# Performance work log

Hardware: AMD Instinct MI355X
Metric: run time of the kernel (lower is better)

The kernel has to match this reference:

```python
import jax, jax.numpy as jnp
import numpy as np

EMBED = 1024
HEADS = 16
HD = EMBED // HEADS
FF = 4096
EPS = 1e-5

def _layernorm(x, g, b):
    mu = jnp.mean(x, axis=-1, keepdims=True)
    var = jnp.mean(jnp.square(x - mu), axis=-1, keepdims=True)
    return (x - mu) * jax.lax.rsqrt(var + EPS) * g + b

def setup_inputs() -> dict:
    key = jax.random.key(0)
    ks = jax.random.split(key, 10)
    s = 0.02
    return {
        "x": jax.random.normal(ks[0], (4, 2048, EMBED), dtype=jnp.float32),
        "Wq": jax.random.normal(ks[1], (EMBED, EMBED), dtype=jnp.float32) * s,
        "Wk": jax.random.normal(ks[2], (EMBED, EMBED), dtype=jnp.float32) * s,
        "Wv": jax.random.normal(ks[3], (EMBED, EMBED), dtype=jnp.float32) * s,
        "Wo": jax.random.normal(ks[4], (EMBED, EMBED), dtype=jnp.float32) * s,
        "bo": jnp.zeros((EMBED,), dtype=jnp.float32),
        "W1": jax.random.normal(ks[5], (EMBED, FF), dtype=jnp.float32) * s,
        "b1": jnp.zeros((FF,), dtype=jnp.float32),
        "W2": jax.random.normal(ks[6], (FF, EMBED), dtype=jnp.float32) * s,
        "b2": jnp.zeros((EMBED,), dtype=jnp.float32),
        "g1": jnp.ones((EMBED,), dtype=jnp.float32),
        "be1": jnp.zeros((EMBED,), dtype=jnp.float32),
        "g2": jnp.ones((EMBED,), dtype=jnp.float32),
        "be2": jnp.zeros((EMBED,), dtype=jnp.float32),
    }

def reference(x, Wq, Wk, Wv, Wo, bo, W1, b1, W2, b2, g1, be1, g2, be2):
    B, T, _ = x.shape
    # --- pre-norm self-attention (dropout = identity in eval) ---
    h = _layernorm(x, g1, be1)
    q = (h @ Wq).reshape(B, T, HEADS, HD).transpose(0, 2, 1, 3)  # bhtd
    k = (h @ Wk).reshape(B, T, HEADS, HD).transpose(0, 2, 1, 3)
    v = (h @ Wv).reshape(B, T, HEADS, HD).transpose(0, 2, 1, 3)
    scores = jnp.einsum('bhid,bhjd->bhij', q, k) / jnp.sqrt(jnp.float32(HD))
    causal = jnp.tril(jnp.ones((T, T), dtype=bool))
    scores = jnp.where(causal[None, None], scores, -jnp.inf)
    attn = jax.nn.softmax(scores, axis=-1)
    out = jnp.einsum('bhij,bhjd->bhid', attn, v)
    out = out.transpose(0, 2, 1, 3).reshape(B, T, EMBED)
    out = out @ Wo + bo
    x = x + out
    # --- pre-norm GELU FFN ---
    h2 = _layernorm(x, g2, be2)
    ff = jax.nn.gelu(h2 @ W1 + b1, approximate=False) @ W2 + b2
    return x + ff
```

## Files before the change

kernel.cpp:

```cpp
#include <hip/hip_runtime.h>

typedef unsigned short u16;
typedef __attribute__((ext_vector_type(8))) short bf16x8;
typedef __attribute__((ext_vector_type(4))) float f32x4;

#define EMBED 1024
#define FFDIM 4096
#define SEQ   2048
#define NTOK  8192
#define ATT_C 0.18033688011112042f

__device__ __forceinline__ u16 f2bf(float f) {
  union { float f; unsigned int u; } c; c.f = f;
  unsigned int r = ((c.u >> 16) & 1u) + 0x7fffu;
  return (u16)((c.u + r) >> 16);
}

__device__ __forceinline__ unsigned cvtpk(float lo, float hi) {
  unsigned r;
  asm("v_cvt_pk_bf16_f32 %0, %1, %2" : "=v"(r) : "v"(lo), "v"(hi));
  return r;
}

__device__ __forceinline__ void gload16(const u16* g, u16* l) {
  __builtin_amdgcn_global_load_lds((const __attribute__((address_space(1))) void*)g,
                                   (__attribute__((address_space(3))) void*)l, 16, 0, 0);
}

__global__ __launch_bounds__(256) void wtrans(const float* __restrict__ W,
                                              u16* __restrict__ Wt, int K, int N) {
  __shared__ float tile[32][33];
  const int tx = threadIdx.x & 31, ty = threadIdx.x >> 5;
  const int n0 = blockIdx.x << 5, k0 = blockIdx.y << 5;
#pragma unroll
  for (int r = 0; r < 32; r += 8)
    tile[ty + r][tx] = W[(size_t)(k0 + ty + r) * N + n0 + tx];
  __syncthreads();
#pragma unroll
  for (int r = 0; r < 32; r += 8)
    Wt[(size_t)(n0 + ty + r) * K + k0 + tx] = f2bf(tile[tx][ty + r]);
}

__global__ __launch_bounds__(256) void vtrans(const u16* __restrict__ qkv,
                                              u16* __restrict__ Vt) {
  __shared__ u16 tile[32][33];
  const int tx = threadIdx.x & 31, ty = threadIdx.x >> 5;
  const int t0 = blockIdx.x << 5;
  const int rg0 = blockIdx.y << 5;
  const int bh = rg0 >> 6, d0 = rg0 & 63;
  const int b = bh >> 4, h = bh & 15;
#pragma unroll
  for (int r = 0; r < 32; r += 8)
    tile[ty + r][tx] = qkv[(size_t)(b * SEQ + t0 + ty + r) * 3072 + 2048 + h * 64 + d0 + tx];
  __syncthreads();
#pragma unroll
  for (int r = 0; r < 32; r += 8)
    Vt[(size_t)(rg0 + ty + r) * SEQ + t0 + tx] = tile[tx][ty + r];
}

__global__ __launch_bounds__(256) void ln_kernel(const float* __restrict__ xin,
                                                 const float* __restrict__ gamma,
                                                 const float* __restrict__ beta,
                                                 u16* __restrict__ out) {
  const int row = blockIdx.x, tid = threadIdx.x;
  const float4 v = reinterpret_cast<const float4*>(xin + (size_t)row * EMBED)[tid];
  float s  = v.x + v.y + v.z + v.w;
  float ss = v.x * v.x + v.y * v.y + v.z * v.z + v.w * v.w;
#pragma unroll
  for (int m = 1; m < 64; m <<= 1) { s += __shfl_xor(s, m); ss += __shfl_xor(ss, m); }
  __shared__ float red[8];
  if ((tid & 63) == 0) { red[tid >> 6] = s; red[4 + (tid >> 6)] = ss; }
  __syncthreads();
  s  = red[0] + red[1] + red[2] + red[3];
  ss = red[4] + red[5] + red[6] + red[7];
  const float mean = s * (1.0f / EMBED);
  const float var  = ss * (1.0f / EMBED) - mean * mean;
  const float rstd = rsqrtf(var + 1e-5f);
  const float4 g  = reinterpret_cast<const float4*>(gamma)[tid];
  const float4 bb = reinterpret_cast<const float4*>(beta)[tid];
  ushort4 o;
  o.x = f2bf((v.x - mean) * rstd * g.x + bb.x);
  o.y = f2bf((v.y - mean) * rstd * g.y + bb.y);
  o.z = f2bf((v.z - mean) * rstd * g.z + bb.z);
  o.w = f2bf((v.w - mean) * rstd * g.w + bb.w);
  reinterpret_cast<ushort4*>(out + (size_t)row * EMBED)[tid] = o;
}

template <int NREP, int EPI>
__global__ __launch_bounds__(512, 2) void gemm4(const u16* __restrict__ A,
                                                const u16* __restrict__ Bt,
                                                void* __restrict__ Cv,
                                                const float* __restrict__ bias,
                                                const float* __restrict__ res,
                                                int M, int N, int K) {
  constexpr int BN = NREP * 64;
  constexpr int G0 = 4;
  constexpr int G1 = (NREP == 4) ? 4 : 3;
  constexpr int G3 = (NREP == 4) ? 4 : 3;
  constexpr int GP = (NREP == 4) ? 4 : 3;
  __shared__ __align__(16) u16 As[2][256 * 64];
  __shared__ __align__(16) u16 Bs[2][BN * 64];

  const int tid = threadIdx.x;
  const int lane = tid & 63, wid = tid >> 6;
  const int l4 = lane >> 4, l15 = lane & 15;
  const int wq = wid >> 2, wn = wid & 3;

  const int gx = gridDim.x;
  const int nwg = gx * (int)gridDim.y;
  const int flat = (int)blockIdx.y * gx + (int)blockIdx.x;
  const int cpx = nwg >> 3;
  const int swz = (flat & 7) * cpx + (flat >> 3);
  const int brow = (swz / gx) << 8;
  const int bcol = (swz % gx) * BN;

  const f32x4 z4 = {0.f, 0.f, 0.f, 0.f};
  f32x4 acc[4][4][NREP / 2];
#pragma unroll
  for (int q = 0; q < 4; ++q)
#pragma unroll
    for (int m = 0; m < 4; ++m)
#pragma unroll
      for (int n = 0; n < NREP / 2; ++n) acc[q][m][n] = z4;

  const int srow = tid >> 3;
  const int scolb = ((tid & 7) << 4) ^ ((srow & 7) << 4);
  const u16* gAs = A  + (size_t)(brow + srow) * K + (scolb >> 1);
  const u16* gBs = Bt + (size_t)(bcol + srow) * K + (scolb >> 1);
  const int lA = wid * 512;

  const int nk = K >> 6;

#define STAGE_A(c_, t_, h_)                                                     \
  do {                                                                          \
    gload16(gAs + (size_t)((h_) * 128) * K + (size_t)(t_) * 64,                 \
            &As[c_][(h_) * 8192 + lA]);                                         \
    gload16(gAs + (size_t)((h_) * 128 + 64) * K + (size_t)(t_) * 64,            \
            &As[c_][(h_) * 8192 + 4096 + lA]);                                  \
  } while (0)
#define STAGE_B(c_, t_, h_)                                                     \
  do {                                                                          \
    if constexpr (NREP == 4) {                                                  \
      gload16(gBs + (size_t)((h_) * 128) * K + (size_t)(t_) * 64,               \
              &Bs[c_][(h_) * 8192 + lA]);                                       \
      gload16(gBs + (size_t)((h_) * 128 + 64) * K + (size_t)(t_) * 64,          \
              &Bs[c_][(h_) * 8192 + 4096 + lA]);                                \
    } else {                                                                    \
      gload16(gBs + (size_t)((h_) * 64) * K + (size_t)(t_) * 64,                \
              &Bs[c_][(h_) * 4096 + lA]);                                       \
    }                                                                           \
  } while (0)

#define SB __builtin_amdgcn_sched_barrier(0)
#define BARR do { SB; __builtin_amdgcn_s_barrier(); SB; } while (0)
#define LG0  do { asm volatile("s_waitcnt lgkmcnt(0)" ::: "memory"); SB; } while (0)
#define VM(N_) do { asm volatile("s_waitcnt vmcnt(%0)" :: "i"(N_) : "memory"); SB; } while (0)

  const int kk0  = l4 << 3;
  const int aswz = (l15 & 7) << 3;

#define RD_A(MH)                                                                \
  _Pragma("unroll")                                                             \
  for (int m_ = 0; m_ < 4; ++m_)                                                \
    _Pragma("unroll")                                                           \
    for (int ks_ = 0; ks_ < 2; ++ks_)                                           \
      af[m_][ks_] = *(const bf16x8*)&As[c][((MH) * 128 + wq * 64 + m_ * 16 + l15) * 64 + ((kk0 + ks_ * 32) ^ aswz)];
#define RD_B(NH)                                                                \
  _Pragma("unroll")                                                             \
  for (int n_ = 0; n_ < NREP / 2; ++n_)                                         \
    _Pragma("unroll")                                                           \
    for (int ks_ = 0; ks_ < 2; ++ks_)                                           \
      bf[n_][ks_] = *(const bf16x8*)&Bs[c][((NH) * (BN / 2) + wn * (BN / 8) + n_ * 16 + l15) * 64 + ((kk0 + ks_ * 32) ^ aswz)];
#define MFMA_Q(Q_)                                                              \
  __builtin_amdgcn_s_setprio(1);                                                \
  _Pragma("unroll")                                                             \
  for (int m_ = 0; m_ < 4; ++m_)                                                \
    _Pragma("unroll")                                                           \
    for (int n_ = 0; n_ < NREP / 2; ++n_)                                       \
      _Pragma("unroll")                                                         \
      for (int ks_ = 0; ks_ < 2; ++ks_)                                         \
        acc[Q_][m_][n_] = __builtin_amdgcn_mfma_f32_16x16x32_bf16(              \
            af[m_][ks_], bf[n_][ks_], acc[Q_][m_][n_], 0, 0, 0);                \
  __builtin_amdgcn_s_setprio(0);

  bf16x8 af[4][2], bf[NREP / 2][2];

  STAGE_A(0, 0, 0);
  STAGE_B(0, 0, 0);
  STAGE_B(0, 0, 1);
  STAGE_A(0, 0, 1);
  VM(GP);
  BARR;

  for (int t = 0; t < nk - 1; ++t) {
    const int c = t & 1, cn = c ^ 1;
    RD_A(0); RD_B(0);
    STAGE_A(cn, t + 1, 0);
    BARR; LG0;
    MFMA_Q(0);
    VM(G0); BARR;
    RD_B(1);
    STAGE_B(cn, t + 1, 0);
    BARR; LG0;
    MFMA_Q(1);
    VM(G1); BARR;
    RD_A(1);
    STAGE_B(cn, t + 1, 1);
    BARR; LG0;
    MFMA_Q(2);
    BARR;
    RD_B(0);
    STAGE_A(cn, t + 1, 1);
    BARR; LG0;
    MFMA_Q(3);
    VM(G3); BARR;
  }

  {
    const int c = (nk - 1) & 1;
    RD_A(0); RD_B(0);
    BARR; LG0;
    MFMA_Q(0);
    VM(2); BARR;
    RD_B(1);
    BARR; LG0;
    MFMA_Q(1);
    VM(0); BARR;
    RD_A(1);
    BARR; LG0;
    MFMA_Q(2);
    BARR;
    RD_B(0);
    LG0;
    MFMA_Q(3);
  }

#undef STAGE_A
#undef STAGE_B
#undef SB
#undef BARR
#undef LG0
#undef VM
#undef RD_A
#undef RD_B
#undef MFMA_Q

#pragma unroll
  for (int q = 0; q < 4; ++q) {
    const int mh = q >> 1, nh = (q >> 1) ^ (q & 1);
    const int rowb = brow + mh * 128 + wq * 64 + (l4 << 2);
    const int colb = bcol + nh * (BN / 2) + wn * (BN / 8) + l15;
#pragma unroll
    for (int n = 0; n < NREP / 2; ++n) {
      const int col = colb + n * 16;
      float bv = 0.f;
      if (EPI != 0) bv = bias[col];
#pragma unroll
      for (int m = 0; m < 4; ++m) {
#pragma unroll
        for (int j = 0; j < 4; ++j) {
          const int row = rowb + m * 16 + j;
          const float v = acc[q][m][n][j];
          if (EPI == 0) {
            ((u16*)Cv)[(size_t)row * N + col] = f2bf(v);
          } else if (EPI == 1) {
            ((float*)Cv)[(size_t)row * N + col] = v + bv + res[(size_t)row * N + col];
          } else {
            const float t2 = v + bv;
            const float gl = 0.5f * t2 * (1.0f + erff(t2 * 0.70710678118654752f));
            ((u16*)Cv)[(size_t)row * N + col] = f2bf(gl);
          }
        }
      }
    }
  }
}

__global__ __launch_bounds__(512) void attn_fwd(const u16* __restrict__ qkv,
                                                const u16* __restrict__ Vt,
                                                u16* __restrict__ attn) {
  __shared__ __align__(16) u16 Ks[64 * 72];
  __shared__ __align__(16) u16 Vs[64 * 72];
  __shared__ __align__(16) u16 Ps[8 * 16 * 72];
  const int tid = threadIdx.x, lane = tid & 63, wid = tid >> 6;
  const int l4 = lane >> 4, l15 = lane & 15;
  const int bh = blockIdx.y, b = bh >> 4, h = bh & 15;
  const size_t bt0 = (size_t)b * SEQ;
  u16* Pw = &Ps[wid * 16 * 72];

  const int sr = tid >> 3;
  const int sc0 = (tid & 7) << 3;
  const u16* kbase = qkv + bt0 * 3072 + 1024 + h * 64;
  const u16* vbase = Vt + (size_t)bh * 64 * SEQ;
  const f32x4 z4 = {0.f, 0.f, 0.f, 0.f};

#pragma unroll
  for (int ph = 0; ph < 2; ++ph) {
    const int Qb = ((ph == 0) ? (int)blockIdx.x : 15 - (int)blockIdx.x) << 7;
    const int qw = Qb + wid * 16;
    const int qlane = qw + l15;

    const u16* qp = qkv + (bt0 + qlane) * 3072 + h * 64 + (l4 << 3);
    const bf16x8 aq0 = *(const bf16x8*)qp;
    const bf16x8 aq1 = *(const bf16x8*)(qp + 32);

    f32x4 o[4];
#pragma unroll
    for (int dt = 0; dt < 4; ++dt) o[dt] = z4;
    float mrun = -1e30f, lrun = 0.f;

    bf16x8 kp = *(const bf16x8*)(kbase + (size_t)sr * 3072 + sc0);
    bf16x8 vp = *(const bf16x8*)(vbase + (size_t)sr * SEQ + sc0);

    const int jend = Qb + 128;
    for (int j0 = 0; j0 < jend; j0 += 64) {
      __syncthreads();
      *(bf16x8*)&Ks[sr * 72 + sc0] = kp;
      *(bf16x8*)&Vs[sr * 72 + sc0] = vp;
      __syncthreads();

      if (j0 + 64 < jend) {
        kp = *(const bf16x8*)(kbase + (size_t)(j0 + 64 + sr) * 3072 + sc0);
        vp = *(const bf16x8*)(vbase + (size_t)sr * SEQ + j0 + 64 + sc0);
      }

      if (j0 > qw + 15) continue;
      const int nt = min(4, ((qw + 15 - j0) >> 4) + 1);

      f32x4 s[4];
#pragma unroll
      for (int t = 0; t < 4; ++t) {
        if (t < nt) {
          const bf16x8 ak0 = *(const bf16x8*)&Ks[(t * 16 + l15) * 72 + (l4 << 3)];
          const bf16x8 ak1 = *(const bf16x8*)&Ks[(t * 16 + l15) * 72 + 32 + (l4 << 3)];
          f32x4 a = z4;
          a = __builtin_amdgcn_mfma_f32_16x16x32_bf16(ak0, aq0, a, 0, 0, 0);
          a = __builtin_amdgcn_mfma_f32_16x16x32_bf16(ak1, aq1, a, 0, 0, 0);
          s[t] = a;
        }
      }

      float mt = -1e30f;
#pragma unroll
      for (int t = 0; t < 4; ++t) {
        if (t < nt) {
          if (j0 + t * 16 + 15 > qw) {
            const int kvb = j0 + t * 16 + (l4 << 2);
#pragma unroll
            for (int j = 0; j < 4; ++j)
              if (kvb + j > qlane) s[t][j] = -1e30f;
          }
          mt = fmaxf(mt, fmaxf(fmaxf(s[t][0], s[t][1]), fmaxf(s[t][2], s[t][3])));
        }
      }
      mt = fmaxf(mt, __shfl_xor(mt, 16));
      mt = fmaxf(mt, __shfl_xor(mt, 32));

      const bool skip = __all(mt <= mrun + 44.0f);
      float scq = 1.0f;
      if (!skip) {
        const float mn = fmaxf(mrun, mt);
        scq = exp2f((mrun - mn) * ATT_C);
        mrun = mn;
      }
      const float mc = mrun * ATT_C;

      float ls = 0.f;
      uint2 pw[4];
#pragma unroll
      for (int t = 0; t < 4; ++t) {
        if (t < nt) {
          const float p0 = exp2f(__builtin_fmaf(s[t][0], ATT_C, -mc));
          const float p1 = exp2f(__builtin_fmaf(s[t][1], ATT_C, -mc));
          const float p2 = exp2f(__builtin_fmaf(s[t][2], ATT_C, -mc));
          const float p3 = exp2f(__builtin_fmaf(s[t][3], ATT_C, -mc));
          ls += (p0 + p1) + (p2 + p3);
          pw[t].x = cvtpk(p0, p1);
          pw[t].y = cvtpk(p2, p3);
        } else {
          pw[t].x = 0u; pw[t].y = 0u;
        }
      }
#pragma unroll
      for (int t = 0; t < 4; ++t)
        *(uint2*)&Pw[l15 * 72 + t * 16 + (l4 << 2)] = pw[t];

      ls += __shfl_xor(ls, 16);
      ls += __shfl_xor(ls, 32);

      if (!skip) {
        lrun = lrun * scq + ls;
#pragma unroll
        for (int dt = 0; dt < 4; ++dt)
#pragma unroll
          for (int j = 0; j < 4; ++j) o[dt][j] *= scq;
      } else {
        lrun += ls;
      }

      const int nc = (nt + 1) >> 1;
#pragma unroll
      for (int c = 0; c < 2; ++c) {
        if (c < nc) {
          const bf16x8 ap = *(const bf16x8*)&Pw[l15 * 72 + c * 32 + (l4 << 3)];
#pragma unroll
          for (int dt = 0; dt < 4; ++dt) {
            const bf16x8 bv = *(const bf16x8*)&Vs[(dt * 16 + l15) * 72 + c * 32 + (l4 << 3)];
            o[dt] = __builtin_amdgcn_mfma_f32_16x16x32_bf16(bv, ap, o[dt], 0, 0, 0);
          }
        }
      }
    }

    const float rl = 1.0f / lrun;
#pragma unroll
    for (int dt = 0; dt < 4; ++dt) {
      uint2 w;
      w.x = cvtpk(o[dt][0] * rl, o[dt][1] * rl);
      w.y = cvtpk(o[dt][2] * rl, o[dt][3] * rl);
      *(uint2*)&Pw[l15 * 72 + dt * 16 + (l4 << 2)] = w;
    }
#pragma unroll
    for (int rep = 0; rep < 2; ++rep) {
      const int unit = rep * 64 + lane;
      const int r = unit >> 3, c = unit & 7;
      const bf16x8 v = *(const bf16x8*)&Pw[r * 72 + c * 8];
      *(bf16x8*)&attn[(bt0 + qw + r) * EMBED + h * 64 + c * 8] = v;
    }
  }
}

extern "C" void kernel_launch(void* const* d_in, const int* in_sizes, int n_in,
                              void* d_out, int out_size, void* d_ws, size_t ws_size,
                              hipStream_t stream) {
  const float* x   = (const float*)d_in[0];
  const float* Wq  = (const float*)d_in[1];
  const float* Wk  = (const float*)d_in[2];
  const float* Wv  = (const float*)d_in[3];
  const float* Wo  = (const float*)d_in[4];
  const float* bo  = (const float*)d_in[5];
  const float* W1  = (const float*)d_in[6];
  const float* b1  = (const float*)d_in[7];
  const float* W2  = (const float*)d_in[8];
  const float* b2  = (const float*)d_in[9];
  const float* g1  = (const float*)d_in[10];
  const float* be1 = (const float*)d_in[11];
  const float* g2  = (const float*)d_in[12];
  const float* be2 = (const float*)d_in[13];

  char* ws = (char*)d_ws;
  u16* wqkv_t = (u16*)(ws + 0);
  u16* wo_t   = (u16*)(ws + 6291456);
  u16* w1_t   = (u16*)(ws + 8388608);
  u16* w2_t   = (u16*)(ws + 16777216);
  u16* hbuf   = (u16*)(ws + 25165824);
  u16* qkv    = (u16*)(ws + 41943040);
  u16* ff1    = (u16*)(ws + 41943040);
  u16* vt     = (u16*)(ws + 92274688);
  u16* attnb  = (u16*)(ws + 109051904);
  float* x2   = (float*)(ws + 125829120);
  float* outp = (float*)d_out;

  dim3 blk(256);
  wtrans<<<dim3(32, 32),  blk, 0, stream>>>(Wq, wqkv_t,               1024, 1024);
  wtrans<<<dim3(32, 32),  blk, 0, stream>>>(Wk, wqkv_t + 1024 * 1024, 1024, 1024);
  wtrans<<<dim3(32, 32),  blk, 0, stream>>>(Wv, wqkv_t + 2048 * 1024, 1024, 1024);
  wtrans<<<dim3(32, 32),  blk, 0, stream>>>(Wo, wo_t,                 1024, 1024);
  wtrans<<<dim3(128, 32), blk, 0, stream>>>(W1, w1_t,                 1024, 4096);
  wtrans<<<dim3(32, 128), blk, 0, stream>>>(W2, w2_t,                 4096, 1024);

  ln_kernel<<<dim3(8192), blk, 0, stream>>>(x, g1, be1, hbuf);
  gemm4<2, 0><<<dim3(24, 32), dim3(512), 0, stream>>>(hbuf, wqkv_t, qkv, nullptr, nullptr,
                                                      8192, 3072, 1024);
  vtrans<<<dim3(64, 128), blk, 0, stream>>>(qkv, vt);
  attn_fwd<<<dim3(8, 64), dim3(512), 0, stream>>>(qkv, vt, attnb);
  gemm4<2, 1><<<dim3(8, 32), dim3(512), 0, stream>>>(attnb, wo_t, x2, bo, x,
                                                     8192, 1024, 1024);
  ln_kernel<<<dim3(8192), blk, 0, stream>>>(x2, g2, be2, hbuf);
  gemm4<4, 2><<<dim3(16, 32), dim3(512), 0, stream>>>(hbuf, w1_t, ff1, b1, nullptr,
                                                      8192, 4096, 1024);
  gemm4<2, 1><<<dim3(8, 32), dim3(512), 0, stream>>>(ff1, w2_t, outp, b2, x2,
                                                     8192, 1024, 4096);
}
```

Measured before the change: 455.9 us.

## Reschedule GEMM pipeline to prefetch two K-tiles ahead with fewer barriers

The GEMM main loop is restructured so global-to-LDS staging for parts of tile t+2 is issued into the current buffer once its quarter has been consumed, and the prologue prefetches part of tile 1. Per-quarter vmcnt waits and the paired sched-barrier fences are replaced by one vmcnt wait per iteration and plain s_barriers, and the separate epilogue iteration is folded into the loop with guards. The aim is deeper overlap of memory loads with MFMA work and fewer synchronisation stalls. It relies on careful reasoning about LDS buffer reuse, so a missed hazard could cause races, and the looser scheduling constraints may let the compiler reorder instructions less favourably.

```diff
diff --git a/kernel.cpp b/kernel.cpp
--- a/kernel.cpp
+++ b/kernel.cpp
@@ -87,16 +87,13 @@
 }
 
 template <int NREP, int EPI>
-__global__ __launch_bounds__(512, 2) void gemm4(const u16* __restrict__ A,
+__global__ __launch_bounds__(512, 2) void gemm5(const u16* __restrict__ A,
                                                 const u16* __restrict__ Bt,
                                                 void* __restrict__ Cv,
                                                 const float* __restrict__ bias,
                                                 const float* __restrict__ res,
                                                 int M, int N, int K) {
   constexpr int BN = NREP * 64;
-  constexpr int G0 = 4;
-  constexpr int G1 = (NREP == 4) ? 4 : 3;
-  constexpr int G3 = (NREP == 4) ? 4 : 3;
   constexpr int GP = (NREP == 4) ? 4 : 3;
   __shared__ __align__(16) u16 As[2][256 * 64];
   __shared__ __align__(16) u16 Bs[2][BN * 64];
@@ -151,11 +148,6 @@
     }                                                                           \
   } while (0)
 
-#define SB __builtin_amdgcn_sched_barrier(0)
-#define BARR do { SB; __builtin_amdgcn_s_barrier(); SB; } while (0)
-#define LG0  do { asm volatile("s_waitcnt lgkmcnt(0)" ::: "memory"); SB; } while (0)
-#define VM(N_) do { asm volatile("s_waitcnt vmcnt(%0)" :: "i"(N_) : "memory"); SB; } while (0)
-
   const int kk0  = l4 << 3;
   const int aswz = (l15 & 7) << 3;
 
@@ -171,6 +163,10 @@
     _Pragma("unroll")                                                           \
     for (int ks_ = 0; ks_ < 2; ++ks_)                                           \
       bf[n_][ks_] = *(const bf16x8*)&Bs[c][((NH) * (BN / 2) + wn * (BN / 8) + n_ * 16 + l15) * 64 + ((kk0 + ks_ * 32) ^ aswz)];
+#define GATE_LG                                                                 \
+  __builtin_amdgcn_s_barrier();                                                 \
+  asm volatile("s_waitcnt lgkmcnt(0)" ::: "memory");                            \
+  __builtin_amdgcn_sched_barrier(0)
 #define MFMA_Q(Q_)                                                              \
   __builtin_amdgcn_s_setprio(1);                                                \
   _Pragma("unroll")                                                             \
@@ -189,60 +185,45 @@
   STAGE_B(0, 0, 0);
   STAGE_B(0, 0, 1);
   STAGE_A(0, 0, 1);
-  VM(GP);
-  BARR;
-
-  for (int t = 0; t < nk - 1; ++t) {
+  if (nk > 1) { STAGE_A(1, 1, 0); STAGE_B(1, 1, 1); }
+  asm volatile("s_waitcnt vmcnt(%0)" :: "i"(GP) : "memory");
+  __builtin_amdgcn_s_barrier();
+
+  for (int t = 0; t < nk; ++t) {
     const int c = t & 1, cn = c ^ 1;
     RD_A(0); RD_B(0);
-    STAGE_A(cn, t + 1, 0);
-    BARR; LG0;
+    if (t + 1 < nk) STAGE_B(cn, t + 1, 0);
+    if constexpr (NREP == 4) asm volatile("s_waitcnt lgkmcnt(8)" ::: "memory");
+    GATE_LG;
     MFMA_Q(0);
-    VM(G0); BARR;
+    __builtin_amdgcn_s_barrier();
     RD_B(1);
-    STAGE_B(cn, t + 1, 0);
-    BARR; LG0;
+    if (t + 1 < nk) STAGE_A(cn, t + 1, 1);
+    GATE_LG;
     MFMA_Q(1);
-    VM(G1); BARR;
+    __builtin_amdgcn_s_barrier();
     RD_A(1);
-    STAGE_B(cn, t + 1, 1);
-    BARR; LG0;
+    if (t + 2 < nk) STAGE_A(c, t + 2, 0);
+    GATE_LG;
     MFMA_Q(2);
-    BARR;
+    __builtin_amdgcn_s_barrier();
     RD_B(0);
-    STAGE_A(cn, t + 1, 1);
-    BARR; LG0;
+    if (t + 2 < nk) STAGE_B(c, t + 2, 1);
+    GATE_LG;
     MFMA_Q(3);
-    VM(G3); BARR;
-  }
-
-  {
-    const int c = (nk - 1) & 1;
-    RD_A(0); RD_B(0);
-    BARR; LG0;
-    MFMA_Q(0);
-    VM(2); BARR;
-    RD_B(1);
-    BARR; LG0;
-    MFMA_Q(1);
-    VM(0); BARR;
-    RD_A(1);
-    BARR; LG0;
-    MFMA_Q(2);
-    BARR;
-    RD_B(0);
-    LG0;
-    MFMA_Q(3);
+    if (t + 2 < nk) {
+      asm volatile("s_waitcnt vmcnt(%0)" :: "i"(GP) : "memory");
+    } else {
+      asm volatile("s_waitcnt vmcnt(0)" ::: "memory");
+    }
+    __builtin_amdgcn_s_barrier();
   }
 
 #undef STAGE_A
 #undef STAGE_B
-#undef SB
-#undef BARR
-#undef LG0
-#undef VM
 #undef RD_A
 #undef RD_B
+#undef GATE_LG
 #undef MFMA_Q
 
 #pragma unroll
@@ -470,15 +451,15 @@
   wtrans<<<dim3(32, 128), blk, 0, stream>>>(W2, w2_t,                 4096, 1024);
 
   ln_kernel<<<dim3(8192), blk, 0, stream>>>(x, g1, be1, hbuf);
-  gemm4<2, 0><<<dim3(24, 32), dim3(512), 0, stream>>>(hbuf, wqkv_t, qkv, nullptr, nullptr,
+  gemm5<2, 0><<<dim3(24, 32), dim3(512), 0, stream>>>(hbuf, wqkv_t, qkv, nullptr, nullptr,
                                                       8192, 3072, 1024);
   vtrans<<<dim3(64, 128), blk, 0, stream>>>(qkv, vt);
   attn_fwd<<<dim3(8, 64), dim3(512), 0, stream>>>(qkv, vt, attnb);
-  gemm4<2, 1><<<dim3(8, 32), dim3(512), 0, stream>>>(attnb, wo_t, x2, bo, x,
+  gemm5<2, 1><<<dim3(8, 32), dim3(512), 0, stream>>>(attnb, wo_t, x2, bo, x,
                                                      8192, 1024, 1024);
   ln_kernel<<<dim3(8192), blk, 0, stream>>>(x2, g2, be2, hbuf);
-  gemm4<4, 2><<<dim3(16, 32), dim3(512), 0, stream>>>(hbuf, w1_t, ff1, b1, nullptr,
+  gemm5<4, 2><<<dim3(16, 32), dim3(512), 0, stream>>>(hbuf, w1_t, ff1, b1, nullptr,
                                                       8192, 4096, 1024);
-  gemm4<2, 1><<<dim3(8, 32), dim3(512), 0, stream>>>(ff1, w2_t, outp, b2, x2,
+  gemm5<2, 1><<<dim3(8, 32), dim3(512), 0, stream>>>(ff1, w2_t, outp, b2, x2,
                                                      8192, 1024, 4096);
 }
```

After: 425.7 us. 1.07x faster.
